# Kernel tuning notes

Measured on AMD Instinct MI355X. Metric: run time of the kernel, lower is better.

The kernel has to match this reference:

```python
import jax, jax.numpy as jnp
import numpy as np

HIDDEN = 1024
OUT = 128
LAYERS = 2
BATCH = 64
SEQ = 1024


def _gru_layer(x_seq, h0, W_ih, W_hh, b_ih, b_hh):
    """x_seq: (B,T,in), h0: (B,H). Returns outputs (B,T,H). PyTorch GRU math."""
    # Precompute input-to-hidden gates once for all timesteps: (B,T,3H)
    gx = jnp.einsum('bti,gi->btg', x_seq, W_ih) + b_ih
    gx = jnp.swapaxes(gx, 0, 1)  # (T,B,3H)

    def step(h, gx_t):
        gh = h @ W_hh.T + b_hh                    # (B,3H)
        xr, xz, xn = jnp.split(gx_t, 3, axis=-1)
        hr, hz, hn = jnp.split(gh, 3, axis=-1)
        r = jax.nn.sigmoid(xr + hr)
        zg = jax.nn.sigmoid(xz + hz)
        n = jnp.tanh(xn + r * hn)
        h_new = (1.0 - zg) * n + zg * h
        return h_new, h_new

    _, ys = jax.lax.scan(step, h0, gx)            # ys: (T,B,H)
    return jnp.swapaxes(ys, 0, 1)                 # (B,T,H)


def setup_inputs() -> dict:
    key = jax.random.key(0)
    ks = jax.random.split(key, 11)
    s = 0.05
    inp = {
        'z': jax.random.normal(ks[0], (BATCH, HIDDEN), dtype=jnp.float32),
        'seq_len': SEQ,
        # layer 0: input size = OUT
        'W_ih_0': jax.random.normal(ks[1], (3 * HIDDEN, OUT), dtype=jnp.float32) * s,
        'W_hh_0': jax.random.normal(ks[2], (3 * HIDDEN, HIDDEN), dtype=jnp.float32) * s,
        'b_ih_0': jax.random.normal(ks[3], (3 * HIDDEN,), dtype=jnp.float32) * s,
        'b_hh_0': jax.random.normal(ks[4], (3 * HIDDEN,), dtype=jnp.float32) * s,
        # layer 1: input size = HIDDEN
        'W_ih_1': jax.random.normal(ks[5], (3 * HIDDEN, HIDDEN), dtype=jnp.float32) * s,
        'W_hh_1': jax.random.normal(ks[6], (3 * HIDDEN, HIDDEN), dtype=jnp.float32) * s,
        'b_ih_1': jax.random.normal(ks[7], (3 * HIDDEN,), dtype=jnp.float32) * s,
        'b_hh_1': jax.random.normal(ks[8], (3 * HIDDEN,), dtype=jnp.float32) * s,
        # output projection
        'W_out': jax.random.normal(ks[9], (OUT, HIDDEN), dtype=jnp.float32) * s,
        'b_out': jax.random.normal(ks[10], (OUT,), dtype=jnp.float32) * s,
    }
    return inp


def reference(z, seq_len, W_ih_0, W_hh_0, b_ih_0, b_hh_0,
              W_ih_1, W_hh_1, b_ih_1, b_hh_1, W_out, b_out):
    B = z.shape[0]
    # hidden = z repeated for each layer; layer 0 input is all zeros
    x0 = jnp.zeros((B, seq_len, OUT), dtype=z.dtype)
    y0 = _gru_layer(x0, z, W_ih_0, W_hh_0, b_ih_0, b_hh_0)   # (B,T,H)
    y1 = _gru_layer(y0, z, W_ih_1, W_hh_1, b_ih_1, b_hh_1)   # (B,T,H)
    reconstructed = jnp.einsum('bth,oh->bto', y1, W_out) + b_out  # (B,T,OUT)
    return reconstructed
```

## Files before the change

kernel.cpp:

```cpp
#include <hip/hip_runtime.h>


#define NBLK 200
#define SMEM_BYTES 152576
#define H 1024
#define T 1024
#define NSLOT 8
#define SLOT(k) (((k) + NSLOT) & (NSLOT - 1))
#define FSTR 32
#define MEMBAR asm volatile("" ::: "memory")

typedef short s16x8 __attribute__((ext_vector_type(8)));
typedef float f32x4 __attribute__((ext_vector_type(4)));
typedef unsigned u32x2 __attribute__((ext_vector_type(2)));

__device__ __forceinline__ unsigned short f2bf(float f) {
  union { float f; unsigned u; } v; v.f = f;
  return (unsigned short)((v.u + 0x7FFFu + ((v.u >> 16) & 1u)) >> 16);
}
__device__ __forceinline__ float sigm(float x) { return 1.f / (1.f + __expf(-x)); }

__device__ __forceinline__ void st_u16(void* p, unsigned short v) {
  __hip_atomic_store((unsigned short*)p, v, __ATOMIC_RELAXED, __HIP_MEMORY_SCOPE_AGENT);
}
__device__ __forceinline__ void st_i32(int* p, int v) {
  __hip_atomic_store(p, v, __ATOMIC_RELAXED, __HIP_MEMORY_SCOPE_AGENT);
}
__device__ __forceinline__ int ld_i32(const int* p) {
  return __hip_atomic_load(p, __ATOMIC_RELAXED, __HIP_MEMORY_SCOPE_AGENT);
}

#define GLD(d, p, off) \
  asm volatile("global_load_dwordx4 %0, %1, off offset:" #off " sc0 sc1" \
               : "=v"(d) : "v"(p))
#define GLDG(A, p) GLD(A[0],p,0); GLD(A[1],p,64); GLD(A[2],p,128); GLD(A[3],p,192)
#define WAITV(n) asm volatile("s_waitcnt vmcnt(" #n ")" ::: "memory")
#define TIE4(A) \
  asm volatile("" : "+v"(A[0]),"+v"(A[1]),"+v"(A[2]),"+v"(A[3]))

__device__ __forceinline__ void gst16f(f32x4 v, void* p) {
  asm volatile("global_store_dwordx4 %0, %1, off sc0 sc1" :: "v"(p), "v"(v) : "memory");
}
__device__ __forceinline__ void gst4(float v, void* p) {
  asm volatile("global_store_dword %0, %1, off sc0 sc1" :: "v"(p), "v"(v) : "memory");
}
__device__ __forceinline__ void gst8u(u32x2 v, void* p) {
  asm volatile("global_store_dwordx2 %0, %1, off sc0 sc1" :: "v"(p), "v"(v) : "memory");
}
__device__ __forceinline__ f32x4 gldf(const float* p) {
  f32x4 d;
  asm volatile("global_load_dwordx4 %0, %1, off sc0 sc1" : "=v"(d) : "v"(p));
  return d;
}

__device__ __forceinline__ void poller(const int* fd, int dtgt,
                                       const int* fgx, int gtgt,
                                       const int* fa, int na, int atgt,
                                       volatile int* ready, int t, int lane) {
  {
    const int* fp = fd + lane * FSTR;
    int v = ld_i32(fp);
    for (;;) {
      int vn = ld_i32(fp);
      unsigned long long m = __ballot(v >= dtgt);
      if (lane < 8 && ((m >> (8 * lane)) & 0xFFull) == 0xFFull) ready[lane] = t;
      if (m == ~0ull) break;
      v = vn;
    }
  }
  if (fgx) {
    int v = (lane == 0) ? ld_i32(fgx) : 0x7fffffff;
    for (;;) {
      int vn = (lane == 0) ? ld_i32(fgx) : 0x7fffffff;
      if (__ballot(v < gtgt) == 0ull) break;
      v = vn;
    }
    if (lane == 0) ready[8] = t;
  }
  if (fa) {
    bool act = lane < na;
    const int* fp = fa + (act ? lane : 0) * FSTR;
    int v = act ? ld_i32(fp) : atgt;
    for (;;) {
      int vn = act ? ld_i32(fp) : atgt;
      if (__ballot(v < atgt) == 0ull) break;
      v = vn;
    }
  }
}

#define MF3(Ap, g) { \
  _Pragma("unroll") \
  for (int i = 0; i < 4; ++i) { int kb = (g)*4 + i; \
    s16x8 b0 = *(const s16x8*)(bb + (kb*3+0)*512); \
    s16x8 b1 = *(const s16x8*)(bb + (kb*3+1)*512); \
    s16x8 b2 = *(const s16x8*)(bb + (kb*3+2)*512); \
    a0 = __builtin_amdgcn_mfma_f32_16x16x32_bf16(Ap[i], b0, a0, 0, 0, 0); \
    a1 = __builtin_amdgcn_mfma_f32_16x16x32_bf16(Ap[i], b1, a1, 0, 0, 0); \
    a2 = __builtin_amdgcn_mfma_f32_16x16x32_bf16(Ap[i], b2, a2, 0, 0, 0); } }

#define MF1(Ap, g) { \
  _Pragma("unroll") \
  for (int i = 0; i < 4; ++i) { int kb = (g)*4 + i; \
    s16x8 b0 = *(const s16x8*)(bb + kb*512); \
    a0 = __builtin_amdgcn_mfma_f32_16x16x32_bf16(Ap[i], b0, a0, 0, 0, 0); } }

__device__ __forceinline__ void gemm48(const unsigned short* arow,
                                       const unsigned short* bb,
                                       volatile int* ready, int t,
                                       float* G, int ldg, int lane, int w) {
  f32x4 a0 = {0,0,0,0}, a1 = {0,0,0,0}, a2 = {0,0,0,0};
  s16x8 A0[4], A1[4];
  while (ready[0] < t) {}
  MEMBAR;
  GLDG(A0, arow);
  while (ready[1] < t) {}
  MEMBAR;
  GLDG(A1, arow + 128);
  #pragma unroll
  for (int g2 = 1; g2 < 4; ++g2) {
    WAITV(4); TIE4(A0); MF3(A0, 2*g2 - 2);
    while (ready[2*g2] < t) {}
    MEMBAR;
    GLDG(A0, arow + g2*256);
    WAITV(4); TIE4(A1); MF3(A1, 2*g2 - 1);
    while (ready[2*g2 + 1] < t) {}
    MEMBAR;
    GLDG(A1, arow + g2*256 + 128);
  }
  WAITV(4); TIE4(A0); MF3(A0, 6);
  WAITV(0); TIE4(A1); MF3(A1, 7);
  int col = lane & 15, r0 = (lane >> 4) * 4;
  #pragma unroll
  for (int r = 0; r < 4; ++r) {
    int brow = w*16 + r0 + r;
    G[brow*ldg +      col] = a0[r];
    G[brow*ldg + 16 + col] = a1[r];
    G[brow*ldg + 32 + col] = a2[r];
  }
}

extern "C" __global__ void __launch_bounds__(512, 1)
gru_pipeline(const float* __restrict__ z,
             const float* __restrict__ Whh0,
             const float* __restrict__ bih0, const float* __restrict__ bhh0,
             const float* __restrict__ Wih1, const float* __restrict__ Whh1,
             const float* __restrict__ bih1, const float* __restrict__ bhh1,
             const float* __restrict__ Wout, const float* __restrict__ bout,
             float* __restrict__ out, char* __restrict__ ws)
{
  extern __shared__ char smem[];
  const int tid  = threadIdx.x;
  const int lane = tid & 63;
  const int w    = tid >> 6;
  const int bid  = blockIdx.x;

  int*            flags = (int*)ws;
  unsigned short* h0    = (unsigned short*)(ws + 32768);
  unsigned short* h1    = (unsigned short*)(ws + 1081344);
  float*          gxw   = (float*)(ws + 2129920);

  int role, p;
  if (bid < 64)       { role = 0; p = bid; }
  else if (bid < 128) { role = 1; p = bid - 64; }
  else if (bid < 192) { role = 2; p = bid - 128; }
  else                { role = 3; p = bid - 192; }
  const int base = p * 16;

  unsigned short* frag = (unsigned short*)smem;
  float* G   = (float*)(smem + 98304);
  float* hm  = (float*)(smem + 123392);
  float* bi  = (float*)(smem + 127488);
  float* bh  = (float*)(smem + 127680);
  volatile int* ready  = (volatile int*)(smem + 127872);
  volatile int* gdone  = (volatile int*)(smem + 127936);
  volatile int* ewflag = (volatile int*)(smem + 127952);
  volatile int* gxst   = (volatile int*)(smem + 127968);
  volatile int* ewdone = (volatile int*)(smem + 127984);
  float* gxl = (float*)(smem + 128000);
  float* bo  = (float*)(smem + 32768);

  int* fS0 = flags;              int* fS1 = flags + 64*FSTR;
  int* fS2 = flags + 128*FSTR;   int* fS3 = flags + 192*FSTR;

  if (tid < 9) ready[tid] = -1;
  if (tid == 0) {
    gdone[0] = gdone[1] = gdone[2] = gdone[3] = -1;
    ewflag[0] = ewflag[1] = ewflag[2] = -1;
    gxst[0] = gxst[1] = gxst[2] = -1;
    *ewdone = -1;
  }
  if (role < 3) {
    const float* W = (role == 0) ? Whh0 : (role == 1) ? Wih1 : Whh1;
    for (int q = tid; q < 6144; q += 512) {
      int c = q % 48; int r2 = q / 48; int grp = r2 & 3; int kb = r2 >> 2;
      int g = c >> 4, u = c & 15;
      unsigned short* dst = frag + (kb*3 + g)*512 + (grp*16 + u)*8;
      const float* s = W + (size_t)(g*H + base + u)*H + kb*32 + grp*8;
      #pragma unroll
      for (int j = 0; j < 8; ++j) dst[j] = f2bf(s[j]);
    }
  }
  if (role == 0 || role == 2) {
    const float* bip = (role == 0) ? bih0 : bih1;
    const float* bhp = (role == 0) ? bhh0 : bhh1;
    if (tid < 48) {
      int g = tid >> 4, u = tid & 15;
      bi[tid] = bip[g*H + base + u];
      bh[tid] = bhp[g*H + base + u];
    }
    unsigned short* hb = (role == 0) ? h0 : h1;
    for (int q = tid; q < 1024; q += 512) {
      int b = q >> 4, u = q & 15;
      float v = z[b*H + base + u];
      hm[q] = v;
      st_u16(&hb[(NSLOT-1)*65536 + b*H + base + u], f2bf(v));
    }
  } else if (role == 3) {
    for (int q = tid; q < 2048; q += 512) {
      int c = q & 15, grp = (q >> 4) & 3, kb = q >> 6;
      unsigned short* dst = frag + kb*512 + (grp*16 + c)*8;
      const float* s = Wout + (size_t)(base + c)*H + kb*32 + grp*8;
      #pragma unroll
      for (int j = 0; j < 8; ++j) dst[j] = f2bf(s[j]);
    }
    if (tid < 16) bo[tid] = bout[base + tid];
  }
  WAITV(0);
  __syncthreads();
  if (tid == 0) st_i32(&flags[(role*64 + p)*FSTR], 1);

  if (role < 3) {
    unsigned short* hsrc = (role == 2) ? h1 : h0;
    if (w < 4) {
      const int ldg = (role == 1) ? 48 : 49;
      const int dt  = (role == 1) ? 0 : 1;
      for (int t = 0; t < 1024; ++t) {
        while (*ewdone < t - 2) {}
        MEMBAR;
        const unsigned short* arow = hsrc + SLOT(t - dt)*65536
                                     + (w*16 + (lane&15))*H + ((lane>>4)*8);
        gemm48(arow, frag + lane*8, ready, t, G + (t&1)*3136, ldg, lane, w);
        MEMBAR;
        gdone[w] = t;
      }
    } else if (w == 7) {
      for (int t = 0; t < 1024; ++t) {
        if (role == 0)      poller(fS0, t+1, nullptr, 0, fS1, 64, t-1, ready, t, lane);
        else if (role == 1) poller(fS0, t+2, nullptr, 0, fS2, 64, t-1, ready, t, lane);
        else                poller(fS2, t+1, &fS1[p*FSTR], t+2, fS3, 8, t-1, ready, t, lane);
      }
    } else {
      const int wv = w - 4;
      const int ewt = wv*64 + lane;
      int* fme = flags + (role*64 + p)*FSTR;
      for (int t = 0; t < 1024; ++t) {
        if (role == 2) {
          while (ready[8] < t) {}
          MEMBAR;
          const float* gxp = gxw + (size_t)(t % 3)*196608 + p*3072
                             + wv*1024 + lane*16;
          f32x4 ga = gldf(gxp), gb = gldf(gxp + 4),
                gc = gldf(gxp + 8), gd = gldf(gxp + 12);
          WAITV(0);
          asm volatile("" : "+v"(ga), "+v"(gb), "+v"(gc), "+v"(gd));
          float* dstl = gxl + (t&1)*3072 + wv*1024 + lane*16;
          *(f32x4*)(dstl)      = ga; *(f32x4*)(dstl + 4)  = gb;
          *(f32x4*)(dstl + 8)  = gc; *(f32x4*)(dstl + 12) = gd;
          MEMBAR;
          gxst[wv] = t;
          while (gxst[0] < t || gxst[1] < t || gxst[2] < t) {}
          MEMBAR;
        }
        while (gdone[0] < t || gdone[1] < t || gdone[2] < t || gdone[3] < t) {}
        MEMBAR;
        float* Gt = G + (t&1)*3136;
        if (role == 1) {
          float* dst = gxw + (size_t)(t % 3)*196608 + p*3072;
          for (int c2 = ewt; c2 < 768; c2 += 192)
            gst16f(*(f32x4*)(Gt + c2*4), dst + c2*4);
        } else {
          float* gx2 = gxl + (t&1)*3072;
          unsigned short* hdst = hsrc + SLOT(t)*65536;
          for (int q = ewt; q < 256; q += 192) {
            int b = q >> 2, u0 = (q & 3) * 4;
            unsigned pk2[2];
            #pragma unroll
            for (int jj = 0; jj < 2; ++jj) {
              unsigned short pk[2];
              #pragma unroll
              for (int j = 0; j < 2; ++j) {
                int u = u0 + jj*2 + j;
                float xr, xz, xn;
                if (role == 0) {
                  xr = bi[u]; xz = bi[16 + u]; xn = bi[32 + u];
                } else {
                  xr = gx2[b*48 + u]      + bi[u];
                  xz = gx2[b*48 + 16 + u] + bi[16 + u];
                  xn = gx2[b*48 + 32 + u] + bi[32 + u];
                }
                float hr = Gt[b*49 + u]      + bh[u];
                float hz = Gt[b*49 + 16 + u] + bh[16 + u];
                float hn = Gt[b*49 + 32 + u] + bh[32 + u];
                float r  = sigm(xr + hr);
                float zg = sigm(xz + hz);
                float n  = tanhf(xn + r * hn);
                int idx = b*16 + u;
                float hp = hm[idx];
                float hv = (1.f - zg) * n + zg * hp;
                hm[idx] = hv;
                pk[j] = f2bf(hv);
              }
              pk2[jj] = (unsigned)pk[0] | ((unsigned)pk[1] << 16);
            }
            u32x2 v2; v2.x = pk2[0]; v2.y = pk2[1];
            gst8u(v2, &hdst[b*H + base + u0]);
          }
        }
        WAITV(0);
        MEMBAR;
        ewflag[wv] = t;
        if (wv == 0) {
          while (ewflag[1] < t || ewflag[2] < t) {}
          MEMBAR;
          if (lane == 0) st_i32(fme, t + 2);
          MEMBAR;
          *ewdone = t;
        }
      }
    }
  } else {
    for (int t = 0; t < 1024; ++t) {
      if (w == 7) {
        poller(fS2, t+2, nullptr, 0, nullptr, 0, 0, ready, t, lane);
      } else if (w < 4) {
        const unsigned short* arow = h1 + (t & (NSLOT-1))*65536
                                     + (w*16 + (lane&15))*H + ((lane>>4)*8);
        const unsigned short* bb = frag + lane*8;
        f32x4 a0 = {0,0,0,0};
        s16x8 A0[4], A1[4];
        while (ready[0] < t) {}
        MEMBAR;
        GLDG(A0, arow);
        while (ready[1] < t) {}
        MEMBAR;
        GLDG(A1, arow + 128);
        #pragma unroll
        for (int g2i = 1; g2i < 4; ++g2i) {
          WAITV(4); TIE4(A0); MF1(A0, 2*g2i - 2);
          while (ready[2*g2i] < t) {}
          MEMBAR;
          GLDG(A0, arow + g2i*256);
          WAITV(4); TIE4(A1); MF1(A1, 2*g2i - 1);
          while (ready[2*g2i + 1] < t) {}
          MEMBAR;
          GLDG(A1, arow + g2i*256 + 128);
        }
        WAITV(4); TIE4(A0); MF1(A0, 6);
        WAITV(0); TIE4(A1); MF1(A1, 7);
        int col = lane & 15, r0 = (lane >> 4) * 4;
        #pragma unroll
        for (int r = 0; r < 4; ++r) {
          int brow = w*16 + r0 + r;
          gst4(a0[r] + bo[col], out + (size_t)(brow*T + t)*128 + base + col);
        }
      }
      WAITV(0);
      __syncthreads();
      if (tid == 0) st_i32(&fS3[p*FSTR], t + 2);
    }
  }
}

extern "C" void kernel_launch(void* const* d_in, const int* in_sizes, int n_in,
                              void* d_out, int out_size, void* d_ws, size_t ws_size,
                              hipStream_t stream) {
  const float* z    = (const float*)d_in[0];
  const float* Whh0 = (const float*)d_in[3];
  const float* bih0 = (const float*)d_in[4];
  const float* bhh0 = (const float*)d_in[5];
  const float* Wih1 = (const float*)d_in[6];
  const float* Whh1 = (const float*)d_in[7];
  const float* bih1 = (const float*)d_in[8];
  const float* bhh1 = (const float*)d_in[9];
  const float* Wout = (const float*)d_in[10];
  const float* bout = (const float*)d_in[11];
  float* out = (float*)d_out;
  char* ws = (char*)d_ws;

  hipFuncSetAttribute((const void*)gru_pipeline,
                      hipFuncAttributeMaxDynamicSharedMemorySize, SMEM_BYTES);
  hipMemsetAsync(d_ws, 0, 32768, stream);

  void* args[] = { (void*)&z, (void*)&Whh0, (void*)&bih0, (void*)&bhh0,
                   (void*)&Wih1, (void*)&Whh1, (void*)&bih1, (void*)&bhh1,
                   (void*)&Wout, (void*)&bout, (void*)&out, (void*)&ws };
  hipLaunchCooperativeKernel((void*)gru_pipeline, dim3(NBLK), dim3(512),
                             args, SMEM_BYTES, stream);
}
```

Measured before the change: 9.820 ms.

## Store layer-1 input gates in bf16 and pipeline flag polling loads

Role-1 blocks now convert the input-gate GEMM results to bf16 before writing them to the global workspace, and role-2 blocks read and stage them in bf16, converting back to fp32 in the elementwise step. This halves the global traffic on the per-step critical path. The flag poller now keeps two loads in flight instead of one. The 'last wave to finish publishes the flag' logic replaces the dedicated wave-0 spin. The bf16 gates add rounding error, and the new publish condition can let several waves write the flag, or none if waves race in a particular order.

Result: slower. 12.48 ms (+27.1%).

```diff
diff --git a/kernel.cpp b/kernel.cpp
--- a/kernel.cpp
+++ b/kernel.cpp
@@ -13,11 +13,15 @@
 typedef short s16x8 __attribute__((ext_vector_type(8)));
 typedef float f32x4 __attribute__((ext_vector_type(4)));
 typedef unsigned u32x2 __attribute__((ext_vector_type(2)));
+typedef int i32x4 __attribute__((ext_vector_type(4)));
 
 __device__ __forceinline__ unsigned short f2bf(float f) {
   union { float f; unsigned u; } v; v.f = f;
   return (unsigned short)((v.u + 0x7FFFu + ((v.u >> 16) & 1u)) >> 16);
 }
+__device__ __forceinline__ float bf2f(unsigned short u) {
+  union { unsigned u; float f; } v; v.u = (unsigned)u << 16; return v.f;
+}
 __device__ __forceinline__ float sigm(float x) { return 1.f / (1.f + __expf(-x)); }
 
 __device__ __forceinline__ void st_u16(void* p, unsigned short v) {
@@ -28,6 +32,11 @@
 }
 __device__ __forceinline__ int ld_i32(const int* p) {
   return __hip_atomic_load(p, __ATOMIC_RELAXED, __HIP_MEMORY_SCOPE_AGENT);
+}
+__device__ __forceinline__ int ldflag(const int* p) {
+  int d;
+  asm volatile("global_load_dword %0, %1, off sc0 sc1" : "=v"(d) : "v"(p));
+  return d;
 }
 
 #define GLD(d, p, off) \
@@ -38,17 +47,14 @@
 #define TIE4(A) \
   asm volatile("" : "+v"(A[0]),"+v"(A[1]),"+v"(A[2]),"+v"(A[3]))
 
-__device__ __forceinline__ void gst16f(f32x4 v, void* p) {
-  asm volatile("global_store_dwordx4 %0, %1, off sc0 sc1" :: "v"(p), "v"(v) : "memory");
-}
 __device__ __forceinline__ void gst4(float v, void* p) {
   asm volatile("global_store_dword %0, %1, off sc0 sc1" :: "v"(p), "v"(v) : "memory");
 }
 __device__ __forceinline__ void gst8u(u32x2 v, void* p) {
   asm volatile("global_store_dwordx2 %0, %1, off sc0 sc1" :: "v"(p), "v"(v) : "memory");
 }
-__device__ __forceinline__ f32x4 gldf(const float* p) {
-  f32x4 d;
+__device__ __forceinline__ i32x4 gldi4(const void* p) {
+  i32x4 d;
   asm volatile("global_load_dwordx4 %0, %1, off sc0 sc1" : "=v"(d) : "v"(p));
   return d;
 }
@@ -59,13 +65,17 @@
                                        volatile int* ready, int t, int lane) {
   {
     const int* fp = fd + lane * FSTR;
-    int v = ld_i32(fp);
+    int f0 = ldflag(fp);
+    int f1 = ldflag(fp);
     for (;;) {
-      int vn = ld_i32(fp);
-      unsigned long long m = __ballot(v >= dtgt);
+      unsigned long long m = __ballot(f0 >= dtgt);
       if (lane < 8 && ((m >> (8 * lane)) & 0xFFull) == 0xFFull) ready[lane] = t;
       if (m == ~0ull) break;
-      v = vn;
+      f0 = ldflag(fp);
+      m = __ballot(f1 >= dtgt);
+      if (lane < 8 && ((m >> (8 * lane)) & 0xFFull) == 0xFFull) ready[lane] = t;
+      if (m == ~0ull) break;
+      f1 = ldflag(fp);
     }
   }
   if (fgx) {
@@ -158,7 +168,7 @@
   int*            flags = (int*)ws;
   unsigned short* h0    = (unsigned short*)(ws + 32768);
   unsigned short* h1    = (unsigned short*)(ws + 1081344);
-  float*          gxw   = (float*)(ws + 2129920);
+  unsigned short* gxw16 = (unsigned short*)(ws + 2129920);
 
   int role, p;
   if (bid < 64)       { role = 0; p = bid; }
@@ -177,7 +187,7 @@
   volatile int* ewflag = (volatile int*)(smem + 127952);
   volatile int* gxst   = (volatile int*)(smem + 127968);
   volatile int* ewdone = (volatile int*)(smem + 127984);
-  float* gxl = (float*)(smem + 128000);
+  unsigned short* gxl16 = (unsigned short*)(smem + 128000);
   float* bo  = (float*)(smem + 32768);
 
   int* fS0 = flags;              int* fS1 = flags + 64*FSTR;
@@ -258,15 +268,14 @@
         if (role == 2) {
           while (ready[8] < t) {}
           MEMBAR;
-          const float* gxp = gxw + (size_t)(t % 3)*196608 + p*3072
-                             + wv*1024 + lane*16;
-          f32x4 ga = gldf(gxp), gb = gldf(gxp + 4),
-                gc = gldf(gxp + 8), gd = gldf(gxp + 12);
+          const unsigned short* gxp = gxw16 + (size_t)(t % 3)*196608 + p*3072
+                                      + wv*1024 + lane*16;
+          i32x4 ga = gldi4(gxp), gb = gldi4(gxp + 8);
           WAITV(0);
-          asm volatile("" : "+v"(ga), "+v"(gb), "+v"(gc), "+v"(gd));
-          float* dstl = gxl + (t&1)*3072 + wv*1024 + lane*16;
-          *(f32x4*)(dstl)      = ga; *(f32x4*)(dstl + 4)  = gb;
-          *(f32x4*)(dstl + 8)  = gc; *(f32x4*)(dstl + 12) = gd;
+          asm volatile("" : "+v"(ga), "+v"(gb));
+          unsigned short* dstl = gxl16 + (t&1)*3072 + wv*1024 + lane*16;
+          *(i32x4*)(dstl)     = ga;
+          *(i32x4*)(dstl + 8) = gb;
           MEMBAR;
           gxst[wv] = t;
           while (gxst[0] < t || gxst[1] < t || gxst[2] < t) {}
@@ -276,11 +285,16 @@
         MEMBAR;
         float* Gt = G + (t&1)*3136;
         if (role == 1) {
-          float* dst = gxw + (size_t)(t % 3)*196608 + p*3072;
-          for (int c2 = ewt; c2 < 768; c2 += 192)
-            gst16f(*(f32x4*)(Gt + c2*4), dst + c2*4);
+          unsigned short* dst = gxw16 + (size_t)(t % 3)*196608 + p*3072;
+          for (int c2 = ewt; c2 < 768; c2 += 192) {
+            f32x4 v = *(f32x4*)(Gt + c2*4);
+            u32x2 d2;
+            d2.x = (unsigned)f2bf(v[0]) | ((unsigned)f2bf(v[1]) << 16);
+            d2.y = (unsigned)f2bf(v[2]) | ((unsigned)f2bf(v[3]) << 16);
+            gst8u(d2, dst + c2*4);
+          }
         } else {
-          float* gx2 = gxl + (t&1)*3072;
+          unsigned short* gx2 = gxl16 + (t&1)*3072;
           unsigned short* hdst = hsrc + SLOT(t)*65536;
           for (int q = ewt; q < 256; q += 192) {
             int b = q >> 2, u0 = (q & 3) * 4;
@@ -295,9 +309,9 @@
                 if (role == 0) {
                   xr = bi[u]; xz = bi[16 + u]; xn = bi[32 + u];
                 } else {
-                  xr = gx2[b*48 + u]      + bi[u];
-                  xz = gx2[b*48 + 16 + u] + bi[16 + u];
-                  xn = gx2[b*48 + 32 + u] + bi[32 + u];
+                  xr = bf2f(gx2[b*48 + u])      + bi[u];
+                  xz = bf2f(gx2[b*48 + 16 + u]) + bi[16 + u];
+                  xn = bf2f(gx2[b*48 + 32 + u]) + bi[32 + u];
                 }
                 float hr = Gt[b*49 + u]      + bh[u];
                 float hz = Gt[b*49 + 16 + u] + bh[16 + u];
@@ -320,9 +334,8 @@
         WAITV(0);
         MEMBAR;
         ewflag[wv] = t;
-        if (wv == 0) {
-          while (ewflag[1] < t || ewflag[2] < t) {}
-          MEMBAR;
+        MEMBAR;
+        if (ewflag[0] >= t && ewflag[1] >= t && ewflag[2] >= t) {
           if (lane == 0) st_i32(fme, t + 2);
           MEMBAR;
           *ewdone = t;
```

## Fuse GRU elementwise into GEMM waves and drop the separate elementwise warps

Applied to the files above, without the earlier changes.

The per-timestep GRU gate math now runs directly on the MFMA accumulators in the four GEMM waves, instead of writing partial sums to shared memory and handing them to three separate elementwise waves. The separate elementwise waves are removed, block size drops from 512 to 320 threads, and the gx staging for layer 1 moves into the single poller wave. Completion flags are now published by whichever GEMM wave sees all four gdone entries, and the output-projection role no longer uses a __syncthreads per step. The aim is to cut shared-memory round trips and intra-block handoff latency on the serial recurrence path. In exchange, hidden-state stores shrink to per-element short stores, and the last-wave-publishes check can race, so a step's flag could be skipped or published twice.

Measured after the change: 8.085 ms. 17.7% less time.

```diff
diff --git a/kernel.cpp b/kernel.cpp
--- a/kernel.cpp
+++ b/kernel.cpp
@@ -2,6 +2,7 @@
 
 
 #define NBLK 200
+#define NTHR 320
 #define SMEM_BYTES 152576
 #define H 1024
 #define T 1024
@@ -12,7 +13,6 @@
 
 typedef short s16x8 __attribute__((ext_vector_type(8)));
 typedef float f32x4 __attribute__((ext_vector_type(4)));
-typedef unsigned u32x2 __attribute__((ext_vector_type(2)));
 
 __device__ __forceinline__ unsigned short f2bf(float f) {
   union { float f; unsigned u; } v; v.f = f;
@@ -38,14 +38,11 @@
 #define TIE4(A) \
   asm volatile("" : "+v"(A[0]),"+v"(A[1]),"+v"(A[2]),"+v"(A[3]))
 
-__device__ __forceinline__ void gst16f(f32x4 v, void* p) {
-  asm volatile("global_store_dwordx4 %0, %1, off sc0 sc1" :: "v"(p), "v"(v) : "memory");
-}
 __device__ __forceinline__ void gst4(float v, void* p) {
   asm volatile("global_store_dword %0, %1, off sc0 sc1" :: "v"(p), "v"(v) : "memory");
 }
-__device__ __forceinline__ void gst8u(u32x2 v, void* p) {
-  asm volatile("global_store_dwordx2 %0, %1, off sc0 sc1" :: "v"(p), "v"(v) : "memory");
+__device__ __forceinline__ void gsts(unsigned short v, void* p) {
+  asm volatile("global_store_short %0, %1, off sc0 sc1" :: "v"(p), "v"((unsigned)v) : "memory");
 }
 __device__ __forceinline__ f32x4 gldf(const float* p) {
   f32x4 d;
@@ -53,39 +50,26 @@
   return d;
 }
 
-__device__ __forceinline__ void poller(const int* fd, int dtgt,
-                                       const int* fgx, int gtgt,
-                                       const int* fa, int na, int atgt,
+__device__ __forceinline__ void pollfd(const int* fd, int dtgt,
                                        volatile int* ready, int t, int lane) {
-  {
-    const int* fp = fd + lane * FSTR;
-    int v = ld_i32(fp);
-    for (;;) {
-      int vn = ld_i32(fp);
-      unsigned long long m = __ballot(v >= dtgt);
-      if (lane < 8 && ((m >> (8 * lane)) & 0xFFull) == 0xFFull) ready[lane] = t;
-      if (m == ~0ull) break;
-      v = vn;
-    }
-  }
-  if (fgx) {
-    int v = (lane == 0) ? ld_i32(fgx) : 0x7fffffff;
-    for (;;) {
-      int vn = (lane == 0) ? ld_i32(fgx) : 0x7fffffff;
-      if (__ballot(v < gtgt) == 0ull) break;
-      v = vn;
-    }
-    if (lane == 0) ready[8] = t;
-  }
-  if (fa) {
-    bool act = lane < na;
-    const int* fp = fa + (act ? lane : 0) * FSTR;
-    int v = act ? ld_i32(fp) : atgt;
-    for (;;) {
-      int vn = act ? ld_i32(fp) : atgt;
-      if (__ballot(v < atgt) == 0ull) break;
-      v = vn;
-    }
+  const int* fp = fd + lane * FSTR;
+  int v = ld_i32(fp);
+  for (;;) {
+    int vn = ld_i32(fp);
+    unsigned long long m = __ballot(v >= dtgt);
+    if (lane < 8 && ((m >> (8 * lane)) & 0xFFull) == 0xFFull) ready[lane] = t;
+    if (m == ~0ull) break;
+    v = vn;
+  }
+}
+__device__ __forceinline__ void pollfa(const int* fa, int na, int atgt, int lane) {
+  bool act = lane < na;
+  const int* fp = fa + (act ? lane : 0) * FSTR;
+  int v = act ? ld_i32(fp) : atgt;
+  for (;;) {
+    int vn = act ? ld_i32(fp) : atgt;
+    if (__ballot(v < atgt) == 0ull) break;
+    v = vn;
   }
 }
 
@@ -105,42 +89,30 @@
     s16x8 b0 = *(const s16x8*)(bb + kb*512); \
     a0 = __builtin_amdgcn_mfma_f32_16x16x32_bf16(Ap[i], b0, a0, 0, 0, 0); } }
 
-__device__ __forceinline__ void gemm48(const unsigned short* arow,
-                                       const unsigned short* bb,
-                                       volatile int* ready, int t,
-                                       float* G, int ldg, int lane, int w) {
-  f32x4 a0 = {0,0,0,0}, a1 = {0,0,0,0}, a2 = {0,0,0,0};
-  s16x8 A0[4], A1[4];
-  while (ready[0] < t) {}
-  MEMBAR;
-  GLDG(A0, arow);
-  while (ready[1] < t) {}
-  MEMBAR;
-  GLDG(A1, arow + 128);
-  #pragma unroll
-  for (int g2 = 1; g2 < 4; ++g2) {
-    WAITV(4); TIE4(A0); MF3(A0, 2*g2 - 2);
-    while (ready[2*g2] < t) {}
-    MEMBAR;
-    GLDG(A0, arow + g2*256);
-    WAITV(4); TIE4(A1); MF3(A1, 2*g2 - 1);
-    while (ready[2*g2 + 1] < t) {}
-    MEMBAR;
-    GLDG(A1, arow + g2*256 + 128);
-  }
-  WAITV(4); TIE4(A0); MF3(A0, 6);
-  WAITV(0); TIE4(A1); MF3(A1, 7);
-  int col = lane & 15, r0 = (lane >> 4) * 4;
-  #pragma unroll
-  for (int r = 0; r < 4; ++r) {
-    int brow = w*16 + r0 + r;
-    G[brow*ldg +      col] = a0[r];
-    G[brow*ldg + 16 + col] = a1[r];
-    G[brow*ldg + 32 + col] = a2[r];
-  }
-}
-
-extern "C" __global__ void __launch_bounds__(512, 1)
+#define GEMM48_BODY(arow) \
+  f32x4 a0 = {0,0,0,0}, a1 = {0,0,0,0}, a2 = {0,0,0,0}; \
+  { s16x8 A0[4], A1[4]; \
+    while (ready[0] < t) {} \
+    MEMBAR; \
+    GLDG(A0, arow); \
+    while (ready[1] < t) {} \
+    MEMBAR; \
+    GLDG(A1, arow + 128); \
+    _Pragma("unroll") \
+    for (int g2 = 1; g2 < 4; ++g2) { \
+      WAITV(4); TIE4(A0); MF3(A0, 2*g2 - 2); \
+      while (ready[2*g2] < t) {} \
+      MEMBAR; \
+      GLDG(A0, arow + g2*256); \
+      WAITV(4); TIE4(A1); MF3(A1, 2*g2 - 1); \
+      while (ready[2*g2 + 1] < t) {} \
+      MEMBAR; \
+      GLDG(A1, arow + g2*256 + 128); \
+    } \
+    WAITV(4); TIE4(A0); MF3(A0, 6); \
+    WAITV(0); TIE4(A1); MF3(A1, 7); }
+
+extern "C" __global__ void __launch_bounds__(NTHR, 1)
 gru_pipeline(const float* __restrict__ z,
              const float* __restrict__ Whh0,
              const float* __restrict__ bih0, const float* __restrict__ bhh0,
@@ -168,15 +140,11 @@
   const int base = p * 16;
 
   unsigned short* frag = (unsigned short*)smem;
-  float* G   = (float*)(smem + 98304);
   float* hm  = (float*)(smem + 123392);
   float* bi  = (float*)(smem + 127488);
   float* bh  = (float*)(smem + 127680);
   volatile int* ready  = (volatile int*)(smem + 127872);
   volatile int* gdone  = (volatile int*)(smem + 127936);
-  volatile int* ewflag = (volatile int*)(smem + 127952);
-  volatile int* gxst   = (volatile int*)(smem + 127968);
-  volatile int* ewdone = (volatile int*)(smem + 127984);
   float* gxl = (float*)(smem + 128000);
   float* bo  = (float*)(smem + 32768);
 
@@ -184,15 +152,10 @@
   int* fS2 = flags + 128*FSTR;   int* fS3 = flags + 192*FSTR;
 
   if (tid < 9) ready[tid] = -1;
-  if (tid == 0) {
-    gdone[0] = gdone[1] = gdone[2] = gdone[3] = -1;
-    ewflag[0] = ewflag[1] = ewflag[2] = -1;
-    gxst[0] = gxst[1] = gxst[2] = -1;
-    *ewdone = -1;
-  }
+  if (tid == 0) { gdone[0] = gdone[1] = gdone[2] = gdone[3] = -1; }
   if (role < 3) {
     const float* W = (role == 0) ? Whh0 : (role == 1) ? Wih1 : Whh1;
-    for (int q = tid; q < 6144; q += 512) {
+    for (int q = tid; q < 6144; q += NTHR) {
       int c = q % 48; int r2 = q / 48; int grp = r2 & 3; int kb = r2 >> 2;
       int g = c >> 4, u = c & 15;
       unsigned short* dst = frag + (kb*3 + g)*512 + (grp*16 + u)*8;
@@ -210,14 +173,14 @@
       bh[tid] = bhp[g*H + base + u];
     }
     unsigned short* hb = (role == 0) ? h0 : h1;
-    for (int q = tid; q < 1024; q += 512) {
+    for (int q = tid; q < 1024; q += NTHR) {
       int b = q >> 4, u = q & 15;
       float v = z[b*H + base + u];
       hm[q] = v;
       st_u16(&hb[(NSLOT-1)*65536 + b*H + base + u], f2bf(v));
     }
   } else if (role == 3) {
-    for (int q = tid; q < 2048; q += 512) {
+    for (int q = tid; q < 2048; q += NTHR) {
       int c = q & 15, grp = (q >> 4) & 3, kb = q >> 6;
       unsigned short* dst = frag + kb*512 + (grp*16 + c)*8;
       const float* s = Wout + (size_t)(base + c)*H + kb*32 + grp*8;
@@ -232,108 +195,102 @@
 
   if (role < 3) {
     unsigned short* hsrc = (role == 2) ? h1 : h0;
-    if (w < 4) {
-      const int ldg = (role == 1) ? 48 : 49;
-      const int dt  = (role == 1) ? 0 : 1;
+    if (w == 4) {
       for (int t = 0; t < 1024; ++t) {
-        while (*ewdone < t - 2) {}
-        MEMBAR;
-        const unsigned short* arow = hsrc + SLOT(t - dt)*65536
-                                     + (w*16 + (lane&15))*H + ((lane>>4)*8);
-        gemm48(arow, frag + lane*8, ready, t, G + (t&1)*3136, ldg, lane, w);
-        MEMBAR;
-        gdone[w] = t;
-      }
-    } else if (w == 7) {
-      for (int t = 0; t < 1024; ++t) {
-        if (role == 0)      poller(fS0, t+1, nullptr, 0, fS1, 64, t-1, ready, t, lane);
-        else if (role == 1) poller(fS0, t+2, nullptr, 0, fS2, 64, t-1, ready, t, lane);
-        else                poller(fS2, t+1, &fS1[p*FSTR], t+2, fS3, 8, t-1, ready, t, lane);
+        if (role == 0) {
+          pollfd(fS0, t+1, ready, t, lane);
+          pollfa(fS1, 64, t-1, lane);
+        } else if (role == 1) {
+          pollfd(fS0, t+2, ready, t, lane);
+          pollfa(fS2, 64, t-1, lane);
+        } else {
+          pollfd(fS2, t+1, ready, t, lane);
+          {
+            int v = (lane == 0) ? ld_i32(&fS1[p*FSTR]) : 0x7fffffff;
+            while (__ballot(v < t+2) != 0ull)
+              v = (lane == 0) ? ld_i32(&fS1[p*FSTR]) : 0x7fffffff;
+          }
+          MEMBAR;
+          const float* gxp = gxw + (size_t)(t % 3)*196608 + p*3072 + lane*48;
+          f32x4 g0 = gldf(gxp),      g1 = gldf(gxp + 4),  g2 = gldf(gxp + 8);
+          f32x4 g3 = gldf(gxp + 12), g4 = gldf(gxp + 16), g5 = gldf(gxp + 20);
+          f32x4 g6 = gldf(gxp + 24), g7 = gldf(gxp + 28), g8 = gldf(gxp + 32);
+          f32x4 g9 = gldf(gxp + 36), ga = gldf(gxp + 40), gb2 = gldf(gxp + 44);
+          WAITV(0);
+          float* dl = gxl + (t&1)*3072 + lane*48;
+          *(f32x4*)(dl)      = g0; *(f32x4*)(dl + 4)  = g1; *(f32x4*)(dl + 8)  = g2;
+          *(f32x4*)(dl + 12) = g3; *(f32x4*)(dl + 16) = g4; *(f32x4*)(dl + 20) = g5;
+          *(f32x4*)(dl + 24) = g6; *(f32x4*)(dl + 28) = g7; *(f32x4*)(dl + 32) = g8;
+          *(f32x4*)(dl + 36) = g9; *(f32x4*)(dl + 40) = ga; *(f32x4*)(dl + 44) = gb2;
+          MEMBAR;
+          if (lane == 0) ready[8] = t;
+          MEMBAR;
+          pollfa(fS3, 8, t-1, lane);
+        }
       }
     } else {
-      const int wv = w - 4;
-      const int ewt = wv*64 + lane;
+      const int dt  = (role == 1) ? 0 : 1;
       int* fme = flags + (role*64 + p)*FSTR;
+      const int col = lane & 15, r0 = (lane >> 4) * 4;
       for (int t = 0; t < 1024; ++t) {
-        if (role == 2) {
-          while (ready[8] < t) {}
-          MEMBAR;
-          const float* gxp = gxw + (size_t)(t % 3)*196608 + p*3072
-                             + wv*1024 + lane*16;
-          f32x4 ga = gldf(gxp), gb = gldf(gxp + 4),
-                gc = gldf(gxp + 8), gd = gldf(gxp + 12);
-          WAITV(0);
-          asm volatile("" : "+v"(ga), "+v"(gb), "+v"(gc), "+v"(gd));
-          float* dstl = gxl + (t&1)*3072 + wv*1024 + lane*16;
-          *(f32x4*)(dstl)      = ga; *(f32x4*)(dstl + 4)  = gb;
-          *(f32x4*)(dstl + 8)  = gc; *(f32x4*)(dstl + 12) = gd;
-          MEMBAR;
-          gxst[wv] = t;
-          while (gxst[0] < t || gxst[1] < t || gxst[2] < t) {}
-          MEMBAR;
-        }
-        while (gdone[0] < t || gdone[1] < t || gdone[2] < t || gdone[3] < t) {}
-        MEMBAR;
-        float* Gt = G + (t&1)*3136;
+        const unsigned short* arow = hsrc + SLOT(t - dt)*65536
+                                     + (w*16 + col)*H + ((lane>>4)*8);
+        const unsigned short* bb = frag + lane*8;
+        GEMM48_BODY(arow);
         if (role == 1) {
           float* dst = gxw + (size_t)(t % 3)*196608 + p*3072;
-          for (int c2 = ewt; c2 < 768; c2 += 192)
-            gst16f(*(f32x4*)(Gt + c2*4), dst + c2*4);
+          #pragma unroll
+          for (int r = 0; r < 4; ++r) {
+            int b = w*16 + r0 + r;
+            gst4(a0[r], dst + b*48 +      col);
+            gst4(a1[r], dst + b*48 + 16 + col);
+            gst4(a2[r], dst + b*48 + 32 + col);
+          }
         } else {
           float* gx2 = gxl + (t&1)*3072;
+          if (role == 2) {
+            while (ready[8] < t) {}
+            MEMBAR;
+          }
           unsigned short* hdst = hsrc + SLOT(t)*65536;
-          for (int q = ewt; q < 256; q += 192) {
-            int b = q >> 2, u0 = (q & 3) * 4;
-            unsigned pk2[2];
-            #pragma unroll
-            for (int jj = 0; jj < 2; ++jj) {
-              unsigned short pk[2];
-              #pragma unroll
-              for (int j = 0; j < 2; ++j) {
-                int u = u0 + jj*2 + j;
-                float xr, xz, xn;
-                if (role == 0) {
-                  xr = bi[u]; xz = bi[16 + u]; xn = bi[32 + u];
-                } else {
-                  xr = gx2[b*48 + u]      + bi[u];
-                  xz = gx2[b*48 + 16 + u] + bi[16 + u];
-                  xn = gx2[b*48 + 32 + u] + bi[32 + u];
-                }
-                float hr = Gt[b*49 + u]      + bh[u];
-                float hz = Gt[b*49 + 16 + u] + bh[16 + u];
-                float hn = Gt[b*49 + 32 + u] + bh[32 + u];
-                float r  = sigm(xr + hr);
-                float zg = sigm(xz + hz);
-                float n  = tanhf(xn + r * hn);
-                int idx = b*16 + u;
-                float hp = hm[idx];
-                float hv = (1.f - zg) * n + zg * hp;
-                hm[idx] = hv;
-                pk[j] = f2bf(hv);
-              }
-              pk2[jj] = (unsigned)pk[0] | ((unsigned)pk[1] << 16);
+          #pragma unroll
+          for (int r = 0; r < 4; ++r) {
+            int b = w*16 + r0 + r;
+            float xr, xz, xn;
+            if (role == 0) {
+              xr = bi[col]; xz = bi[16 + col]; xn = bi[32 + col];
+            } else {
+              xr = gx2[b*48 +      col] + bi[col];
+              xz = gx2[b*48 + 16 + col] + bi[16 + col];
+              xn = gx2[b*48 + 32 + col] + bi[32 + col];
             }
-            u32x2 v2; v2.x = pk2[0]; v2.y = pk2[1];
-            gst8u(v2, &hdst[b*H + base + u0]);
+            float hr = a0[r] + bh[col];
+            float hz = a1[r] + bh[16 + col];
+            float hn = a2[r] + bh[32 + col];
+            float rg = sigm(xr + hr);
+            float zg = sigm(xz + hz);
+            float n  = tanhf(xn + rg * hn);
+            int idx = b*16 + col;
+            float hp = hm[idx];
+            float hv = (1.f - zg) * n + zg * hp;
+            hm[idx] = hv;
+            gsts(f2bf(hv), &hdst[b*H + base + col]);
           }
         }
         WAITV(0);
         MEMBAR;
-        ewflag[wv] = t;
-        if (wv == 0) {
-          while (ewflag[1] < t || ewflag[2] < t) {}
-          MEMBAR;
+        gdone[w] = t;
+        MEMBAR;
+        if (gdone[0] >= t && gdone[1] >= t && gdone[2] >= t && gdone[3] >= t) {
           if (lane == 0) st_i32(fme, t + 2);
-          MEMBAR;
-          *ewdone = t;
         }
       }
     }
   } else {
     for (int t = 0; t < 1024; ++t) {
-      if (w == 7) {
-        poller(fS2, t+2, nullptr, 0, nullptr, 0, 0, ready, t, lane);
-      } else if (w < 4) {
+      if (w == 4) {
+        pollfd(fS2, t+2, ready, t, lane);
+      } else {
         const unsigned short* arow = h1 + (t & (NSLOT-1))*65536
                                      + (w*16 + (lane&15))*H + ((lane>>4)*8);
         const unsigned short* bb = frag + lane*8;
@@ -364,10 +321,14 @@
           int brow = w*16 + r0 + r;
           gst4(a0[r] + bo[col], out + (size_t)(brow*T + t)*128 + base + col);
         }
+        WAITV(0);
+        MEMBAR;
+        gdone[w] = t;
+        MEMBAR;
+        if (gdone[0] >= t && gdone[1] >= t && gdone[2] >= t && gdone[3] >= t) {
+          if (lane == 0) st_i32(&fS3[p*FSTR], t + 2);
+        }
       }
-      WAITV(0);
-      __syncthreads();
-      if (tid == 0) st_i32(&fS3[p*FSTR], t + 2);
     }
   }
 }
@@ -395,6 +356,6 @@
   void* args[] = { (void*)&z, (void*)&Whh0, (void*)&bih0, (void*)&bhh0,
                    (void*)&Wih1, (void*)&Whh1, (void*)&bih1, (void*)&bhh1,
                    (void*)&Wout, (void*)&bout, (void*)&out, (void*)&ws };
-  hipLaunchCooperativeKernel((void*)gru_pipeline, dim3(NBLK), dim3(512),
+  hipLaunchCooperativeKernel((void*)gru_pipeline, dim3(NBLK), dim3(NTHR),
                              args, SMEM_BYTES, stream);
 }
```
